# Kernel optimization log

Measured on AMD Instinct MI355X. Metric: run time of the kernel, lower is better.

The kernel has to match this reference:

```python
import jax, jax.numpy as jnp
import numpy as np

UP = 2
KSIZE = 3
RES = 64
LRELU_SLOPE = 0.2
ACT_GAIN = float(np.sqrt(2.0))  # def_gain of 'lrelu' in bias_act


def _setup_filter():
    # upfirdn2d.setup_filter([1,3,3,1]): normalize, make separable 2D filter
    f = jnp.array([1.0, 3.0, 3.0, 1.0], dtype=jnp.float32)
    f = f / jnp.sum(f)
    return jnp.outer(f, f)  # [4,4]


def _upfirdn2d_up2(x, f2):
    # Zero-insertion upsample by 2 + pad + FIR filter, gain = up**2.
    # Torch path: zero-insert to 2H, pad (3,2), conv 4-tap -> 2H+2.
    # lhs_dilation gives 2H-1; absorbing the trailing inserted zero into the
    # right pad ((3,3) instead of (3,2)) is exactly equivalent.
    B, C, H, W = x.shape
    k = (f2 * (UP * UP)).astype(x.dtype)[None, None]  # [1,1,4,4] (symmetric, flip-invariant)
    k = jnp.tile(k, (C, 1, 1, 1))                     # depthwise [C,1,4,4]
    return jax.lax.conv_general_dilated(
        x, k, window_strides=(1, 1), padding=((3, 3), (3, 3)),
        lhs_dilation=(UP, UP),
        dimension_numbers=('NCHW', 'OIHW', 'NCHW'),
        feature_group_count=C)


def setup_inputs() -> dict:
    key = jax.random.key(0)
    ks = jax.random.split(key, 6)
    B, Cin, Cout, Wd = 16, 512, 512, 512
    Hin = RES // UP
    return {
        "x": jax.random.normal(ks[0], (B, Cin, Hin, Hin), jnp.float32),
        "w": jax.random.normal(ks[1], (B, Wd), jnp.float32),
        "affine_weight": jax.random.normal(ks[2], (Cin, Wd), jnp.float32),
        "affine_bias": jnp.ones((Cin,), jnp.float32),  # bias_init=1
        "weight": jax.random.normal(ks[3], (Cout, Cin, KSIZE, KSIZE), jnp.float32),
        "bias": jnp.zeros((Cout,), jnp.float32),
        "noise_const": jax.random.normal(ks[4], (RES, RES), jnp.float32),
        "noise_strength": jax.random.uniform(ks[5], (), jnp.float32),
    }


def reference(x, w, affine_weight, affine_bias, weight, bias, noise_const, noise_strength):
    B, Cin, Hin, Win = x.shape
    Cout = weight.shape[0]
    # affine: FullyConnectedLayer, weight_gain = 1/sqrt(w_dim), bias_init=1
    styles = w @ affine_weight.T * (1.0 / np.sqrt(w.shape[1])) + affine_bias  # [B,Cin]
    # modulate + demodulate (fused_modconv=True): per-sample weights
    wmod = weight[None] * styles[:, None, :, None, None]                     # [B,Cout,Cin,kh,kw]
    dcoef = jax.lax.rsqrt(jnp.sum(jnp.square(wmod), axis=(2, 3, 4)) + 1e-8)  # [B,Cout]
    wmod = wmod * dcoef[:, :, None, None, None]
    # up=2 -> flip_weight=False -> true convolution: flip spatial taps
    wmod = wmod[..., ::-1, ::-1]
    # conv2d_resample: upfirdn2d upsample first (pad = k//2 + (fw+up-1)//2 = 3), then VALID conv
    xu = _upfirdn2d_up2(x, _setup_filter())                                  # [B,Cin,66,66]
    xr = xu.reshape(1, B * Cin, xu.shape[2], xu.shape[3])
    wr = wmod.reshape(B * Cout, Cin, KSIZE, KSIZE)
    y = jax.lax.conv_general_dilated(
        xr, wr, window_strides=(1, 1), padding='VALID',
        dimension_numbers=('NCHW', 'OIHW', 'NCHW'),
        feature_group_count=B)
    y = y.reshape(B, Cout, RES, RES)
    # noise_mode='const': noise = noise_const * noise_strength
    y = y + noise_const * noise_strength
    # fused bias + lrelu + def_gain (gain=1, conv_clamp=None)
    y = jax.nn.leaky_relu(y + bias[None, :, None, None], LRELU_SLOPE) * ACT_GAIN
    return y
```

## Files before the change

kernel.cpp:

```cpp
#include <hip/hip_runtime.h>
#include <hip/hip_bf16.h>
#include <math.h>

#define CIN   512
#define COUT  512
#define NB    16
#define WD    512
#define HIN   32
#define HUP   66
#define RES   64
#define LRELU 0.2f
#define ACT_GAIN 1.4142135623730951f

typedef __attribute__((ext_vector_type(8))) short short8;
typedef __attribute__((ext_vector_type(4))) float float4v;

__global__ void styles2_kernel(const float* __restrict__ w,
                               const float* __restrict__ aw,
                               const float* __restrict__ ab,
                               float* __restrict__ styles) {
    int b = blockIdx.x;
    int cig = blockIdx.y;
    int lane = threadIdx.x & 63, wv = threadIdx.x >> 6;
    __shared__ float wsh[WD];
    for (int e = threadIdx.x; e < WD; e += 256) wsh[e] = w[b * WD + e];
    __syncthreads();
    for (int r = 0; r < 16; ++r) {
        int ci = cig * 64 + wv * 16 + r;
        const float* arow = aw + (size_t)ci * WD;
        float acc = 0.f;
        for (int k = lane; k < WD; k += 64) acc += arow[k] * wsh[k];
        for (int off = 32; off; off >>= 1) acc += __shfl_down(acc, off, 64);
        if (lane == 0)
            styles[b * CIN + ci] = acc * 0.04419417382415922f + ab[ci];
    }
}

__global__ void prep_weights(const float* __restrict__ weight,
                             float* __restrict__ wsq,
                             __hip_bfloat16* __restrict__ wb) {
    int idx = blockIdx.x * 256 + threadIdx.x;
    int co = idx & (COUT - 1);
    int ci = idx >> 9;
    const float* wp = weight + ((size_t)co * CIN + ci) * 9;
    int cc = ci >> 5, chi = (ci >> 3) & 3, clo = ci & 7;
    float s = 0.f;
#pragma unroll
    for (int t = 0; t < 9; ++t) {
        float v = wp[t];
        s += v * v;
        int tf = 8 - t;
        wb[((((size_t)cc * 9 + tf) * 4 + chi) * COUT + co) * 8 + clo] = __float2bfloat16(v);
    }
    wsq[(size_t)co * CIN + ci] = s;
}

__global__ void dcoef2_kernel(const float* __restrict__ styles,
                              const float* __restrict__ wsq,
                              float* __restrict__ dcoef) {
    int b = blockIdx.x;
    int cog = blockIdx.y;
    int lane = threadIdx.x & 63, wv = threadIdx.x >> 6;
    __shared__ float s2[CIN];
    for (int e = threadIdx.x; e < CIN; e += 256) {
        float s = styles[b * CIN + e];
        s2[e] = s * s;
    }
    __syncthreads();
    for (int r = 0; r < 16; ++r) {
        int co = cog * 64 + wv * 16 + r;
        const float* qrow = wsq + (size_t)co * CIN;
        float acc = 0.f;
        for (int k = lane; k < CIN; k += 64) acc += qrow[k] * s2[k];
        for (int off = 32; off; off >>= 1) acc += __shfl_down(acc, off, 64);
        if (lane == 0) dcoef[b * COUT + co] = rsqrtf(acc + 1e-8f);
    }
}

__global__ void upmod2_kernel(const float* __restrict__ x,
                              const float* __restrict__ styles,
                              __hip_bfloat16* __restrict__ xs2) {
    __shared__ float xt[128 * 65];
    const int oh = blockIdx.x;
    const int ci0 = blockIdx.y * 128;
    const int b = blockIdx.z;
    int m0, m1; float a0, a1;
    if (oh & 1) { m0 = (oh - 3) >> 1; a0 = 0.125f; m1 = (oh - 1) >> 1; a1 = 0.375f; }
    else        { m0 = (oh >> 1) - 1; a0 = 0.375f; m1 = (oh >> 1);     a1 = 0.125f; }
    for (int e = threadIdx.x; e < 8192; e += 256) {
        int ci = e >> 6, sel = (e >> 5) & 1, iw = e & 31;
        int m = sel ? m1 : m0;
        float v = 0.f;
        if (m >= 0 && m < HIN)
            v = x[((size_t)(b * CIN + ci0 + ci) * HIN + m) * HIN + iw];
        xt[ci * 65 + sel * 32 + iw] = v;
    }
    __syncthreads();
    for (int e = threadIdx.x; e < 66 * 128; e += 256) {
        int ci = e & 127, ow = e >> 7;
        int n0i, n1i; float b0, b1;
        if (ow & 1) { n0i = (ow - 3) >> 1; b0 = 0.125f; n1i = (ow - 1) >> 1; b1 = 0.375f; }
        else        { n0i = (ow >> 1) - 1; b0 = 0.375f; n1i = (ow >> 1);     b1 = 0.125f; }
        bool c0 = (n0i >= 0) & (n0i < HIN);
        bool c1 = (n1i >= 0) & (n1i < HIN);
        float r0 = (c0 ? xt[ci * 65 + n0i] : 0.f) * b0 + (c1 ? xt[ci * 65 + n1i] : 0.f) * b1;
        float r1 = (c0 ? xt[ci * 65 + 32 + n0i] : 0.f) * b0 + (c1 ? xt[ci * 65 + 32 + n1i] : 0.f) * b1;
        float s = styles[b * CIN + ci0 + ci] * 4.0f;
        float val = (a0 * r0 + a1 * r1) * s;
        xs2[(((size_t)b * HUP + oh) * HUP + ow) * CIN + ci0 + ci] = __float2bfloat16(val);
    }
}

#define LDA_SZ 25600
#define LDB_SZ 36864

__global__ __launch_bounds__(256, 2) void conv_mfma(
        const __hip_bfloat16* __restrict__ xs2,
        const __hip_bfloat16* __restrict__ wb,
        const float* __restrict__ dcoef,
        const float* __restrict__ bias,
        const float* __restrict__ noise,
        const float* __restrict__ nstr,
        float* __restrict__ out)
{
    __shared__ __align__(16) char smem[LDA_SZ + LDB_SZ];
    const int tid = threadIdx.x;
    const int lane = tid & 63;
    const int wid = tid >> 6;
    const int li = lane & 15;
    const int q = lane >> 4;
    const int mt = blockIdx.x;
    const int n0 = blockIdx.y * 64;
    const int b  = blockIdx.z;
    const int y0 = mt * 4;

    long a_goff[7];
    int  a_lds[7];
#pragma unroll
    for (int k = 0; k < 7; ++k) {
        int n = wid + k * 4;
        if (n < 25) {
            int s = n * 64 + lane;
            if (s > 1583) s = 1583;
            int r = s / 264;
            int rem = s - r * 264;
            int chi = rem / 66;
            int col = rem - chi * 66;
            a_goff[k] = ((long)(b * HUP + y0 + r) * HUP + col) * CIN + chi * 8;
            a_lds[k] = n * 1024;
        } else { a_goff[k] = 0; a_lds[k] = -1; }
    }
    long b_goff[9];
#pragma unroll
    for (int k = 0; k < 9; ++k) {
        int sl = wid + k * 4;
        b_goff[k] = ((long)sl * COUT + n0) * 8 + (long)lane * 8;
    }

    float4v acc[4][4];
#pragma unroll
    for (int i = 0; i < 4; ++i)
#pragma unroll
        for (int j = 0; j < 4; ++j) acc[i][j] = (float4v)0.f;

    const char* xg = (const char*)xs2;
    const char* wg = (const char*)wb;

    for (int cc = 0; cc < 16; ++cc) {
#pragma unroll
        for (int k = 0; k < 9; ++k) {
            int sl = wid + k * 4;
            long ge = (long)cc * 147456 + b_goff[k];
            __builtin_amdgcn_global_load_lds(
                (const __attribute__((address_space(1))) char*)(wg + ge * 2),
                (__attribute__((address_space(3))) char*)(smem + LDA_SZ + sl * 1024),
                16, 0, 0);
        }
#pragma unroll
        for (int k = 0; k < 7; ++k) {
            if (a_lds[k] >= 0) {
                long ge = a_goff[k] + (long)cc * 32;
                __builtin_amdgcn_global_load_lds(
                    (const __attribute__((address_space(1))) char*)(xg + ge * 2),
                    (__attribute__((address_space(3))) char*)(smem + a_lds[k]),
                    16, 0, 0);
            }
        }
        __syncthreads();

#pragma unroll
        for (int t = 0; t < 9; ++t) {
            const int kh = t / 3, kw = t - kh * 3;
            short8 bf[4];
#pragma unroll
            for (int j = 0; j < 4; ++j)
                bf[j] = *(const short8*)(smem + LDA_SZ +
                        (((t * 4 + q) * 64) + j * 16 + li) * 16);
#pragma unroll
            for (int i = 0; i < 4; ++i) {
                short8 af = *(const short8*)(smem +
                        ((((wid + kh) * 4 + q) * 66) + (i * 16 + li + kw)) * 16);
#pragma unroll
                for (int j = 0; j < 4; ++j)
                    acc[i][j] = __builtin_amdgcn_mfma_f32_16x16x32_bf16(
                        af, bf[j], acc[i][j], 0, 0, 0);
            }
        }
        __syncthreads();
    }

    const float ns = nstr[0];
    const int row = y0 + wid;
#pragma unroll
    for (int j = 0; j < 4; ++j) {
        int cout = n0 + j * 16 + li;
        float dc = dcoef[b * COUT + cout];
        float bs = bias[cout];
        float* op = out + ((size_t)(b * COUT + cout) * RES + row) * RES;
#pragma unroll
        for (int i = 0; i < 4; ++i) {
            int colb = i * 16 + q * 4;
            float4v nz = *(const float4v*)(noise + row * RES + colb);
            float4v a = acc[i][j];
            float4v r;
            r.x = a.x * dc + nz.x * ns + bs;
            r.y = a.y * dc + nz.y * ns + bs;
            r.z = a.z * dc + nz.z * ns + bs;
            r.w = a.w * dc + nz.w * ns + bs;
            r.x = (r.x > 0.f ? r.x : LRELU * r.x) * ACT_GAIN;
            r.y = (r.y > 0.f ? r.y : LRELU * r.y) * ACT_GAIN;
            r.z = (r.z > 0.f ? r.z : LRELU * r.z) * ACT_GAIN;
            r.w = (r.w > 0.f ? r.w : LRELU * r.w) * ACT_GAIN;
            *(float4v*)(op + colb) = r;
        }
    }
}

extern "C" void kernel_launch(void* const* d_in, const int* in_sizes, int n_in,
                              void* d_out, int out_size, void* d_ws, size_t ws_size,
                              hipStream_t stream) {
    (void)in_sizes; (void)n_in; (void)out_size; (void)ws_size;
    const float* x     = (const float*)d_in[0];
    const float* w     = (const float*)d_in[1];
    const float* aw    = (const float*)d_in[2];
    const float* ab    = (const float*)d_in[3];
    const float* wt    = (const float*)d_in[4];
    const float* bias  = (const float*)d_in[5];
    const float* noise = (const float*)d_in[6];
    const float* nstr  = (const float*)d_in[7];
    float* out = (float*)d_out;

    char* ws = (char*)d_ws;
    float* styles = (float*)ws;
    float* dcoef  = (float*)(ws + 32768);
    float* wsq    = (float*)(ws + 65536);
    __hip_bfloat16* wb  = (__hip_bfloat16*)(ws + 65536 + 1048576);
    __hip_bfloat16* xs2 = (__hip_bfloat16*)(ws + 65536 + 1048576 + 4718592);

    styles2_kernel<<<dim3(NB, 8), dim3(256), 0, stream>>>(w, aw, ab, styles);
    prep_weights<<<dim3(1024), dim3(256), 0, stream>>>(wt, wsq, wb);
    dcoef2_kernel<<<dim3(NB, 8), dim3(256), 0, stream>>>(styles, wsq, dcoef);
    upmod2_kernel<<<dim3(HUP, 4, NB), dim3(256), 0, stream>>>(x, styles, xs2);
    conv_mfma<<<dim3(16, 8, NB), dim3(256), 0, stream>>>(
        xs2, wb, dcoef, bias, noise, nstr, out);
}
```

Before: 542.9 us.

## Prefetch next K-chunk into registers while computing current chunk's MFMAs

Replaces the direct global-to-LDS loads, which were issued and then waited on before every chunk's compute, with register prefetching. The loads for chunk cc+1 are issued before the MFMA loop for chunk cc and written to LDS after a barrier, so global memory latency overlaps with matrix math. It also raises wave priority around the MFMA block. The cost is extra VGPR pressure from holding up to 16 float4 registers, which may lower occupancy, plus an added barrier per iteration.

```diff
diff --git a/kernel.cpp b/kernel.cpp
--- a/kernel.cpp
+++ b/kernel.cpp
@@ -166,28 +166,40 @@
     const char* xg = (const char*)xs2;
     const char* wg = (const char*)wb;
 
+    float4v rA[7];
+    float4v rB[9];
+
+#define ISSUE_LOADS(CC) do {                                                  \
+        long ccl_ = (long)(CC);                                               \
+        _Pragma("unroll")                                                     \
+        for (int k = 0; k < 9; ++k)                                           \
+            rB[k] = *(const float4v*)(wg + (ccl_ * 147456 + b_goff[k]) * 2);  \
+        _Pragma("unroll")                                                     \
+        for (int k = 0; k < 7; ++k)                                           \
+            if (a_lds[k] >= 0)                                                \
+                rA[k] = *(const float4v*)(xg + (a_goff[k] + ccl_ * 32) * 2);  \
+    } while (0)
+
+#define WRITE_LDS() do {                                                      \
+        _Pragma("unroll")                                                     \
+        for (int k = 0; k < 9; ++k)                                           \
+            *(float4v*)(smem + LDA_SZ + (wid + k * 4) * 1024 + lane * 16)     \
+                = rB[k];                                                      \
+        _Pragma("unroll")                                                     \
+        for (int k = 0; k < 7; ++k)                                           \
+            if (a_lds[k] >= 0)                                                \
+                *(float4v*)(smem + a_lds[k] + lane * 16) = rA[k];             \
+    } while (0)
+
+    ISSUE_LOADS(0);
+    WRITE_LDS();
+    __syncthreads();
+
     for (int cc = 0; cc < 16; ++cc) {
-#pragma unroll
-        for (int k = 0; k < 9; ++k) {
-            int sl = wid + k * 4;
-            long ge = (long)cc * 147456 + b_goff[k];
-            __builtin_amdgcn_global_load_lds(
-                (const __attribute__((address_space(1))) char*)(wg + ge * 2),
-                (__attribute__((address_space(3))) char*)(smem + LDA_SZ + sl * 1024),
-                16, 0, 0);
-        }
-#pragma unroll
-        for (int k = 0; k < 7; ++k) {
-            if (a_lds[k] >= 0) {
-                long ge = a_goff[k] + (long)cc * 32;
-                __builtin_amdgcn_global_load_lds(
-                    (const __attribute__((address_space(1))) char*)(xg + ge * 2),
-                    (__attribute__((address_space(3))) char*)(smem + a_lds[k]),
-                    16, 0, 0);
-            }
-        }
-        __syncthreads();
-
+        if (cc < 15) ISSUE_LOADS(cc + 1);
+        __builtin_amdgcn_sched_barrier(0);
+
+        __builtin_amdgcn_s_setprio(1);
 #pragma unroll
         for (int t = 0; t < 9; ++t) {
             const int kh = t / 3, kw = t - kh * 3;
@@ -206,8 +218,17 @@
                         af, bf[j], acc[i][j], 0, 0, 0);
             }
         }
+        __builtin_amdgcn_s_setprio(0);
+
         __syncthreads();
-    }
+        if (cc < 15) {
+            WRITE_LDS();
+            __syncthreads();
+        }
+    }
+
+#undef ISSUE_LOADS
+#undef WRITE_LDS
 
     const float ns = nstr[0];
     const int row = y0 + wid;
```

Result: slower. 558.7 us (+2.9%).

## Double conv output tile rows, pad LDS weight layout, vectorize upsample kernel

Applied to the files above, without the earlier changes.

The conv kernel now covers 8 output rows per block instead of 4, and each wave accumulates two rows (8x4 MFMA tiles). This halves the grid and reuses each loaded weight slice across twice as many pixels, cutting redundant weight traffic. The weight LDS layout gets padded strides, likely to reduce bank conflicts, and dynamic shared memory (~81KB) is enabled via hipFuncSetAttribute. The upsample kernel now loads float4, caches styles in LDS and writes 8 bf16 channels per store. Costs are higher register and LDS pressure, which may lower occupancy below the 2 blocks/CU requested by launch bounds.

```diff
diff --git a/kernel.cpp b/kernel.cpp
--- a/kernel.cpp
+++ b/kernel.cpp
@@ -80,39 +80,51 @@
 __global__ void upmod2_kernel(const float* __restrict__ x,
                               const float* __restrict__ styles,
                               __hip_bfloat16* __restrict__ xs2) {
-    __shared__ float xt[128 * 65];
+    __shared__ float xt[128 * 68];
+    __shared__ float ssh[128];
     const int oh = blockIdx.x;
     const int ci0 = blockIdx.y * 128;
     const int b = blockIdx.z;
     int m0, m1; float a0, a1;
     if (oh & 1) { m0 = (oh - 3) >> 1; a0 = 0.125f; m1 = (oh - 1) >> 1; a1 = 0.375f; }
     else        { m0 = (oh >> 1) - 1; a0 = 0.375f; m1 = (oh >> 1);     a1 = 0.125f; }
-    for (int e = threadIdx.x; e < 8192; e += 256) {
-        int ci = e >> 6, sel = (e >> 5) & 1, iw = e & 31;
+    if (threadIdx.x < 128) ssh[threadIdx.x] = styles[b * CIN + ci0 + threadIdx.x] * 4.0f;
+    for (int e = threadIdx.x; e < 2048; e += 256) {
+        int ci = e >> 4, sel = (e >> 3) & 1, iw4 = e & 7;
         int m = sel ? m1 : m0;
-        float v = 0.f;
+        float4v v = (float4v)0.f;
         if (m >= 0 && m < HIN)
-            v = x[((size_t)(b * CIN + ci0 + ci) * HIN + m) * HIN + iw];
-        xt[ci * 65 + sel * 32 + iw] = v;
+            v = *(const float4v*)(x + ((size_t)(b * CIN + ci0 + ci) * HIN + m) * HIN + iw4 * 4);
+        *(float4v*)(&xt[ci * 68 + sel * 32 + iw4 * 4]) = v;
     }
     __syncthreads();
-    for (int e = threadIdx.x; e < 66 * 128; e += 256) {
-        int ci = e & 127, ow = e >> 7;
+    for (int e = threadIdx.x; e < 1056; e += 256) {
+        int cig = e / 66;
+        int ow = e - cig * 66;
         int n0i, n1i; float b0, b1;
         if (ow & 1) { n0i = (ow - 3) >> 1; b0 = 0.125f; n1i = (ow - 1) >> 1; b1 = 0.375f; }
         else        { n0i = (ow >> 1) - 1; b0 = 0.375f; n1i = (ow >> 1);     b1 = 0.125f; }
         bool c0 = (n0i >= 0) & (n0i < HIN);
         bool c1 = (n1i >= 0) & (n1i < HIN);
-        float r0 = (c0 ? xt[ci * 65 + n0i] : 0.f) * b0 + (c1 ? xt[ci * 65 + n1i] : 0.f) * b1;
-        float r1 = (c0 ? xt[ci * 65 + 32 + n0i] : 0.f) * b0 + (c1 ? xt[ci * 65 + 32 + n1i] : 0.f) * b1;
-        float s = styles[b * CIN + ci0 + ci] * 4.0f;
-        float val = (a0 * r0 + a1 * r1) * s;
-        xs2[(((size_t)b * HUP + oh) * HUP + ow) * CIN + ci0 + ci] = __float2bfloat16(val);
-    }
-}
-
-#define LDA_SZ 25600
-#define LDB_SZ 36864
+        short8 sv;
+#pragma unroll
+        for (int u = 0; u < 8; ++u) {
+            int ci = cig * 8 + u;
+            const float* base = &xt[ci * 68];
+            float r0 = (c0 ? base[n0i] : 0.f) * b0 + (c1 ? base[n1i] : 0.f) * b1;
+            float r1 = (c0 ? base[32 + n0i] : 0.f) * b0 + (c1 ? base[32 + n1i] : 0.f) * b1;
+            float val = (a0 * r0 + a1 * r1) * ssh[ci];
+            __hip_bfloat16 h = __float2bfloat16(val);
+            sv[u] = *reinterpret_cast<const short*>(&h);
+        }
+        *reinterpret_cast<short8*>(
+            xs2 + (((size_t)b * HUP + oh) * HUP + ow) * CIN + ci0 + cig * 8) = sv;
+    }
+}
+
+#define LDA_SZ 43008
+#define LDB_SZ 38016
+#define LDS_TOT (LDA_SZ + LDB_SZ)
 
 __global__ __launch_bounds__(256, 2) void conv_mfma(
         const __hip_bfloat16* __restrict__ xs2,
@@ -123,43 +135,44 @@
         const float* __restrict__ nstr,
         float* __restrict__ out)
 {
-    __shared__ __align__(16) char smem[LDA_SZ + LDB_SZ];
+    extern __shared__ __align__(16) char smem[];
     const int tid = threadIdx.x;
     const int lane = tid & 63;
     const int wid = tid >> 6;
     const int li = lane & 15;
     const int q = lane >> 4;
-    const int mt = blockIdx.x;
+    const int mb = blockIdx.x;
     const int n0 = blockIdx.y * 64;
     const int b  = blockIdx.z;
-    const int y0 = mt * 4;
-
-    long a_goff[7];
-    int  a_lds[7];
-#pragma unroll
-    for (int k = 0; k < 7; ++k) {
+    const int y0 = mb * 8;
+
+    int a_goff[11];
+    int a_lds[11];
+#pragma unroll
+    for (int k = 0; k < 11; ++k) {
         int n = wid + k * 4;
-        if (n < 25) {
+        if (n < 42) {
             int s = n * 64 + lane;
-            if (s > 1583) s = 1583;
+            if (s > 2639) s = 2639;
             int r = s / 264;
             int rem = s - r * 264;
             int chi = rem / 66;
             int col = rem - chi * 66;
-            a_goff[k] = ((long)(b * HUP + y0 + r) * HUP + col) * CIN + chi * 8;
+            a_goff[k] = ((b * HUP + y0 + r) * HUP + col) * CIN + chi * 8;
             a_lds[k] = n * 1024;
         } else { a_goff[k] = 0; a_lds[k] = -1; }
     }
-    long b_goff[9];
+    int b_goff[9], b_lds[9];
 #pragma unroll
     for (int k = 0; k < 9; ++k) {
         int sl = wid + k * 4;
-        b_goff[k] = ((long)sl * COUT + n0) * 8 + (long)lane * 8;
-    }
-
-    float4v acc[4][4];
-#pragma unroll
-    for (int i = 0; i < 4; ++i)
+        b_goff[k] = (sl * COUT + n0 + lane) * 8;
+        b_lds[k] = LDA_SZ + (sl >> 2) * 4224 + (sl & 3) * 1056;
+    }
+
+    float4v acc[8][4];
+#pragma unroll
+    for (int i = 0; i < 8; ++i)
 #pragma unroll
         for (int j = 0; j < 4; ++j) acc[i][j] = (float4v)0.f;
 
@@ -169,17 +182,16 @@
     for (int cc = 0; cc < 16; ++cc) {
 #pragma unroll
         for (int k = 0; k < 9; ++k) {
-            int sl = wid + k * 4;
-            long ge = (long)cc * 147456 + b_goff[k];
+            long ge = (long)(b_goff[k] + cc * 147456);
             __builtin_amdgcn_global_load_lds(
                 (const __attribute__((address_space(1))) char*)(wg + ge * 2),
-                (__attribute__((address_space(3))) char*)(smem + LDA_SZ + sl * 1024),
+                (__attribute__((address_space(3))) char*)(smem + b_lds[k]),
                 16, 0, 0);
         }
 #pragma unroll
-        for (int k = 0; k < 7; ++k) {
+        for (int k = 0; k < 11; ++k) {
             if (a_lds[k] >= 0) {
-                long ge = a_goff[k] + (long)cc * 32;
+                long ge = (long)(a_goff[k] + cc * 32);
                 __builtin_amdgcn_global_load_lds(
                     (const __attribute__((address_space(1))) char*)(xg + ge * 2),
                     (__attribute__((address_space(3))) char*)(smem + a_lds[k]),
@@ -194,12 +206,13 @@
             short8 bf[4];
 #pragma unroll
             for (int j = 0; j < 4; ++j)
-                bf[j] = *(const short8*)(smem + LDA_SZ +
-                        (((t * 4 + q) * 64) + j * 16 + li) * 16);
-#pragma unroll
-            for (int i = 0; i < 4; ++i) {
+                bf[j] = *(const short8*)(smem + LDA_SZ + t * 4224 + q * 1056 +
+                                         (j * 16 + li) * 16);
+#pragma unroll
+            for (int i = 0; i < 8; ++i) {
+                int rl = wid * 2 + (i >> 2) + kh;
                 short8 af = *(const short8*)(smem +
-                        ((((wid + kh) * 4 + q) * 66) + (i * 16 + li + kw)) * 16);
+                        ((rl * 4 + q) * 66 + ((i & 3) * 16 + li + kw)) * 16);
 #pragma unroll
                 for (int j = 0; j < 4; ++j)
                     acc[i][j] = __builtin_amdgcn_mfma_f32_16x16x32_bf16(
@@ -210,16 +223,16 @@
     }
 
     const float ns = nstr[0];
-    const int row = y0 + wid;
 #pragma unroll
     for (int j = 0; j < 4; ++j) {
         int cout = n0 + j * 16 + li;
         float dc = dcoef[b * COUT + cout];
         float bs = bias[cout];
-        float* op = out + ((size_t)(b * COUT + cout) * RES + row) * RES;
-#pragma unroll
-        for (int i = 0; i < 4; ++i) {
-            int colb = i * 16 + q * 4;
+#pragma unroll
+        for (int i = 0; i < 8; ++i) {
+            int row = y0 + wid * 2 + (i >> 2);
+            int colb = (i & 3) * 16 + q * 4;
+            float* op = out + ((size_t)(b * COUT + cout) * RES + row) * RES + colb;
             float4v nz = *(const float4v*)(noise + row * RES + colb);
             float4v a = acc[i][j];
             float4v r;
@@ -231,7 +244,7 @@
             r.y = (r.y > 0.f ? r.y : LRELU * r.y) * ACT_GAIN;
             r.z = (r.z > 0.f ? r.z : LRELU * r.z) * ACT_GAIN;
             r.w = (r.w > 0.f ? r.w : LRELU * r.w) * ACT_GAIN;
-            *(float4v*)(op + colb) = r;
+            *(float4v*)op = r;
         }
     }
 }
@@ -250,6 +263,13 @@
     const float* nstr  = (const float*)d_in[7];
     float* out = (float*)d_out;
 
+    static bool init = false;
+    if (!init) {
+        hipFuncSetAttribute(reinterpret_cast<const void*>(conv_mfma),
+                            hipFuncAttributeMaxDynamicSharedMemorySize, LDS_TOT);
+        init = true;
+    }
+
     char* ws = (char*)d_ws;
     float* styles = (float*)ws;
     float* dcoef  = (float*)(ws + 32768);
@@ -261,6 +281,6 @@
     prep_weights<<<dim3(1024), dim3(256), 0, stream>>>(wt, wsq, wb);
     dcoef2_kernel<<<dim3(NB, 8), dim3(256), 0, stream>>>(styles, wsq, dcoef);
     upmod2_kernel<<<dim3(HUP, 4, NB), dim3(256), 0, stream>>>(x, styles, xs2);
-    conv_mfma<<<dim3(16, 8, NB), dim3(256), 0, stream>>>(
+    conv_mfma<<<dim3(8, 8, NB), dim3(256), LDS_TOT, stream>>>(
         xs2, wb, dcoef, bias, noise, nstr, out);
 }
```

New measurement: 523.9 us. 1.04x faster.
